# Optimization experiments

Measured on AMD Instinct MI355X. Metric: run time of the kernel, lower is better.

## Reference

```python
import jax, jax.numpy as jnp
import numpy as np

N = 4096   # num nodes
D = 512    # hidden_dim
H = 8      # head_num (hardcoded in module)
E = 131072 # num relation pairs
DH = D // H


def setup_inputs() -> dict:
    key = jax.random.key(0)
    k1, k2, k3, k4, k5, k6 = jax.random.split(key, 6)
    inst_feature = jax.random.normal(k1, (N, D), jnp.float32)
    aggregator_matrix = jax.random.randint(k2, (N, N), 0, 2).astype(jnp.float32)
    # unique (sub, obj) pairs to avoid nondeterministic duplicate scatter-set
    rng = np.random.default_rng(0)
    flat = rng.choice(N * N, size=E, replace=False)
    rel_pair_index = jnp.stack(
        [jnp.asarray(flat // N, jnp.int32), jnp.asarray(flat % N, jnp.int32)], axis=1)
    std = np.sqrt(2.0 / (D + DH)).astype(np.float32)
    w_q = jax.random.normal(k3, (D, D), jnp.float32) * std
    w_k = jax.random.normal(k4, (D, D), jnp.float32) * std
    bnd = 1.0 / np.sqrt(D)
    b_q = jax.random.uniform(k5, (D,), jnp.float32, -bnd, bnd)
    b_k = jax.random.uniform(k6, (D,), jnp.float32, -bnd, bnd)
    return {"inst_feature": inst_feature, "aggregator_matrix": aggregator_matrix,
            "rel_pair_index": rel_pair_index, "w_q": w_q, "b_q": b_q,
            "w_k": w_k, "b_k": b_k}


def reference(inst_feature, aggregator_matrix, rel_pair_index, w_q, b_q, w_k, b_k):
    n, d = inst_feature.shape
    sub = rel_pair_index[:, 0]
    obj = rel_pair_index[:, 1]
    # gather + project (eval mode: dropouts are identity)
    q = (inst_feature[sub] @ w_q.T + b_q).reshape(-1, H, DH)  # [E,H,dh]
    k = (inst_feature[obj] @ w_k.T + b_k).reshape(-1, H, DH)  # [E,H,dh]
    scores = (q * k).sum(-1) / np.sqrt(DH).astype(np.float32)  # [E,H]
    # scatter into dense [H,N,N]
    af = jnp.zeros((H, n, n), inst_feature.dtype).at[:, sub, obj].set(scores.T)
    # mask where aggregator_matrix == 0 (applied before diagonal override)
    af = jnp.where((aggregator_matrix == 0)[None], -jnp.inf, af)
    diag = jnp.arange(n)
    af = af.at[:, diag, diag].set(1e-7)
    p = jax.nn.softmax(af, axis=2)          # softmax over last dim
    factor = p.sum(axis=0) / H              # [N,N]
    return factor @ inst_feature            # [N,D]
```

## Files before the change

### kernel.cpp

```cpp
#include <hip/hip_runtime.h>

#define N_INST 4096
#define D_FEAT 512
#define NHEAD 8
#define NPAIR 131072

typedef __attribute__((ext_vector_type(8))) short short8;
typedef __attribute__((ext_vector_type(4))) float f32x4;
typedef __attribute__((ext_vector_type(4))) unsigned short u16x4;

__device__ inline unsigned short f2bf(float f) {
  union { float f; unsigned u; } v; v.f = f;
  unsigned r = v.u + 0x7fffu + ((v.u >> 16) & 1u);
  return (unsigned short)(r >> 16);
}
__device__ inline float bf2f(unsigned short b) {
  union { unsigned u; float f; } v; v.u = ((unsigned)b) << 16; return v.f;
}
__device__ inline void gload16(const void* g, void* l) {
  __builtin_amdgcn_global_load_lds((const __attribute__((address_space(1))) unsigned int*)g,
                                   (__attribute__((address_space(3))) unsigned int*)l, 16, 0, 0);
}

__global__ __launch_bounds__(256) void k_castw(const float* __restrict__ wq,
                                               const float* __restrict__ wk,
                                               unsigned short* __restrict__ dst) {
  const float* src = blockIdx.y ? wk : wq;
  unsigned short* d = dst + (size_t)blockIdx.y * D_FEAT * D_FEAT;
  int i = (blockIdx.x * 256 + threadIdx.x) * 4;
  float4 v = *(const float4*)&src[i];
  ushort4 o;
  o.x = f2bf(v.x); o.y = f2bf(v.y); o.z = f2bf(v.z); o.w = f2bf(v.w);
  *(ushort4*)&d[i] = o;
}

__global__ __launch_bounds__(256) void k_xprep(const float* __restrict__ x,
                                               unsigned short* __restrict__ xb,
                                               unsigned short* __restrict__ xT) {
  __shared__ float t[32][33];
  int bx = blockIdx.x, by = blockIdx.y;
  int tx = threadIdx.x & 31, ty = threadIdx.x >> 5;
  #pragma unroll
  for (int r = 0; r < 4; ++r) {
    int row = by * 32 + ty + r * 8;
    float v = x[(size_t)row * D_FEAT + bx * 32 + tx];
    t[ty + r * 8][tx] = v;
    xb[(size_t)row * D_FEAT + bx * 32 + tx] = f2bf(v);
  }
  __syncthreads();
  #pragma unroll
  for (int r = 0; r < 4; ++r)
    xT[(size_t)(bx * 32 + ty + r * 8) * N_INST + by * 32 + tx] = f2bf(t[tx][ty + r * 8]);
}

__global__ __launch_bounds__(256) void k_mask_acnt(const float* __restrict__ agg,
                                                   unsigned short* __restrict__ maskb,
                                                   int* __restrict__ acnt) {
  int i = blockIdx.x;
  const f32x4* row = (const f32x4*)(agg + (size_t)i * N_INST);
  u16x4* mrow = (u16x4*)(maskb + (size_t)i * N_INST);
  int tid = threadIdx.x;
  f32x4 v[4];
  #pragma unroll
  for (int u = 0; u < 4; ++u)
    v[u] = __builtin_nontemporal_load(&row[u * 256 + tid]);
  int cnt = 0;
  #pragma unroll
  for (int u = 0; u < 4; ++u) {
    int t = u * 256 + tid;
    u16x4 m;
    m[0] = (v[u][0] != 0.f) ? 0x3F80 : 0;
    m[1] = (v[u][1] != 0.f) ? 0x3F80 : 0;
    m[2] = (v[u][2] != 0.f) ? 0x3F80 : 0;
    m[3] = (v[u][3] != 0.f) ? 0x3F80 : 0;
    cnt += (v[u][0] != 0.f) + (v[u][1] != 0.f) + (v[u][2] != 0.f) + (v[u][3] != 0.f);
    int j = t * 4;
    if (i >= j && i < j + 4) {
      int d = i - j;
      m[d] = 0x3F80;
      cnt -= (v[u][d] != 0.f);
    }
    __builtin_nontemporal_store(m, &mrow[t]);
  }
  #pragma unroll
  for (int msk = 1; msk < 64; msk <<= 1) cnt += __shfl_xor(cnt, msk);
  __shared__ int wsum[4];
  if ((threadIdx.x & 63) == 0) wsum[threadIdx.x >> 6] = cnt;
  __syncthreads();
  if (threadIdx.x == 0) acnt[i] = wsum[0] + wsum[1] + wsum[2] + wsum[3];
}

template<int BIAS, int CBF16, int BN>
__global__ __launch_bounds__(256, 2) void k_gemm(const unsigned short* __restrict__ A,
                                                 const unsigned short* __restrict__ B,
                                                 const float* __restrict__ bias0,
                                                 const float* __restrict__ bias1,
                                                 void* __restrict__ Cv,
                                                 int M, int N, int K, int klen) {
  constexpr int NI = BN / 32;
  constexpr int BCH = BN / 32;
  __shared__ __align__(16) unsigned short lA[2][128 * 64];
  __shared__ __align__(16) unsigned short lB[2][BN * 64];
  int tid = threadIdx.x, wave = tid >> 6, lane = tid & 63;
  int wm = wave & 1, wn = wave >> 1;
  int gx = gridDim.x;
  int nxy = gx * gridDim.y;
  int lin = blockIdx.x + gx * blockIdx.y;
  int nch = nxy >> 3;
  int nl = (lin & 7) * nch + (lin >> 3);
  int bx = nl % gx, by = nl / gx;
  int bm = by * 128, bn = bx * BN;
  int kbase = blockIdx.z * klen;
  int srow = lane >> 3;
  int sg = (lane & 7) ^ srow;
  const unsigned short* ag[4];
  const unsigned short* bg[BCH];
  #pragma unroll
  for (int p = 0; p < 4; ++p) {
    int row = (wave * 4 + p) * 8 + srow;
    ag[p] = A + (size_t)(bm + row) * K + kbase + sg * 8;
  }
  #pragma unroll
  for (int p = 0; p < BCH; ++p) {
    int row = (wave * BCH + p) * 8 + srow;
    bg[p] = B + (size_t)(bn + row) * K + kbase + sg * 8;
  }
  auto stage = [&](int buf) {
    #pragma unroll
    for (int p = 0; p < 4; ++p) { gload16(ag[p], &lA[buf][(wave * 4 + p) * 512]); ag[p] += 64; }
    #pragma unroll
    for (int p = 0; p < BCH; ++p) { gload16(bg[p], &lB[buf][(wave * BCH + p) * 512]); bg[p] += 64; }
  };
  f32x4 acc[4][NI] = {};
  int nt = klen / 64;
  stage(0);
  __syncthreads();
  int cur = 0;
  int lrow = lane & 15, glq = lane >> 4;
  for (int t = 0; t < nt; ++t) {
    if (t + 1 < nt) stage(cur ^ 1);
    short8 bf[2][NI];
    #pragma unroll
    for (int kk = 0; kk < 2; ++kk)
      #pragma unroll
      for (int ni = 0; ni < NI; ++ni) {
        int row = wn * (BN / 2) + ni * 16 + lrow;
        int pg = (kk * 4 + glq) ^ (row & 7);
        bf[kk][ni] = *(const short8*)&lB[cur][row * 64 + pg * 8];
      }
    #pragma unroll
    for (int mi = 0; mi < 4; ++mi)
      #pragma unroll
      for (int kk = 0; kk < 2; ++kk) {
        int row = wm * 64 + mi * 16 + lrow;
        int pg = (kk * 4 + glq) ^ (row & 7);
        short8 af = *(const short8*)&lA[cur][row * 64 + pg * 8];
        #pragma unroll
        for (int ni = 0; ni < NI; ++ni)
          acc[mi][ni] = __builtin_amdgcn_mfma_f32_16x16x32_bf16(af, bf[kk][ni], acc[mi][ni], 0, 0, 0);
      }
    __syncthreads();
    cur ^= 1;
  }
  #pragma unroll
  for (int mi = 0; mi < 4; ++mi)
    #pragma unroll
    for (int ni = 0; ni < NI; ++ni) {
      int col = bn + wn * (BN / 2) + ni * 16 + lrow;
      float bv = 0.f;
      if (BIAS) bv = (col < 512) ? bias0[col] : bias1[col - 512];
      #pragma unroll
      for (int j = 0; j < 4; ++j) {
        int row = bm + wm * 64 + mi * 16 + glq * 4 + j;
        float vv = acc[mi][ni][j] + bv;
        if (CBF16) {
          ((unsigned short*)Cv)[(size_t)row * N + col] = f2bf(vv);
        } else {
          float* C = (float*)Cv + (size_t)blockIdx.z * M * N;
          C[(size_t)row * N + col] = vv;
        }
      }
    }
}

__global__ __launch_bounds__(256) void k_scores(const unsigned short* __restrict__ QKb,
                                                const int* __restrict__ pairs,
                                                const float* __restrict__ agg,
                                                float* __restrict__ es,
                                                float* __restrict__ sumexp,
                                                int* __restrict__ scnt) {
  int wave = threadIdx.x >> 6, lane = threadIdx.x & 63;
  int e = blockIdx.x * 4 + wave;
  int sub = pairs[2 * e], obj = pairs[2 * e + 1];
  short8 q8 = *(const short8*)&QKb[(size_t)sub * 1024 + lane * 8];
  short8 k8 = *(const short8*)&QKb[(size_t)obj * 1024 + 512 + lane * 8];
  float p = 0.f;
  #pragma unroll
  for (int j = 0; j < 8; ++j)
    p += bf2f((unsigned short)q8[j]) * bf2f((unsigned short)k8[j]);
  p += __shfl_xor(p, 1);
  p += __shfl_xor(p, 2);
  p += __shfl_xor(p, 4);
  float ev = expf(p * 0.125f);
  bool valid = (sub != obj) && (agg[(size_t)sub * N_INST + obj] != 0.f);
  int h = lane >> 3;
  if ((lane & 7) == 0) {
    es[(size_t)e * 8 + h] = valid ? ev : -1.f;
    if (valid) atomicAdd(&sumexp[sub * 8 + h], ev);
  }
  if (lane == 0 && valid) atomicAdd(&scnt[sub], 1);
}

__global__ __launch_bounds__(256) void k_denom(const float* __restrict__ sumexp,
                                               const int* __restrict__ scnt,
                                               const int* __restrict__ acnt,
                                               float* __restrict__ invden,
                                               float* __restrict__ base) {
  int i = blockIdx.x * 256 + threadIdx.x;
  if (i >= N_INST) return;
  float c0 = (float)(acnt[i] - scnt[i]);
  const float E0 = expf(1e-7f);
  float bsum = 0.f;
  #pragma unroll
  for (int h = 0; h < NHEAD; ++h) {
    float inv = 1.0f / (E0 + c0 + sumexp[i * NHEAD + h]);
    invden[i * NHEAD + h] = inv;
    bsum += inv;
  }
  base[i] = bsum * (1.0f / NHEAD);
}

__global__ __launch_bounds__(256) void k_scatter(const int* __restrict__ pairs,
                                                 const float* __restrict__ es,
                                                 const float* __restrict__ invden,
                                                 const float* __restrict__ base,
                                                 unsigned short* __restrict__ maskb) {
  int e = blockIdx.x * 256 + threadIdx.x;
  if (e >= NPAIR) return;
  float4 e0 = *(const float4*)&es[(size_t)e * 8];
  if (e0.x < 0.f) return;
  float4 e1 = *(const float4*)&es[(size_t)e * 8 + 4];
  int sub = pairs[2 * e], obj = pairs[2 * e + 1];
  const float* inv = &invden[sub * 8];
  float f = e0.x * inv[0] + e0.y * inv[1] + e0.z * inv[2] + e0.w * inv[3] +
            e1.x * inv[4] + e1.y * inv[5] + e1.z * inv[6] + e1.w * inv[7];
  maskb[(size_t)sub * N_INST + obj] = f2bf(f * 0.125f / base[sub]);
}

__global__ __launch_bounds__(256) void k_redscale(const float* __restrict__ P,
                                                  const float* __restrict__ base,
                                                  float* __restrict__ out) {
  size_t idx = ((size_t)blockIdx.x * 256 + threadIdx.x) * 4;
  int i = (int)(idx >> 9);
  const size_t S = (size_t)N_INST * 512;
  float4 a = *(const float4*)&P[idx];
  float4 b = *(const float4*)&P[idx + S];
  float4 c = *(const float4*)&P[idx + 2 * S];
  float4 d = *(const float4*)&P[idx + 3 * S];
  float s = base[i];
  float4 o;
  o.x = s * (a.x + b.x + c.x + d.x);
  o.y = s * (a.y + b.y + c.y + d.y);
  o.z = s * (a.z + b.z + c.z + d.z);
  o.w = s * (a.w + b.w + c.w + d.w);
  *(float4*)&out[idx] = o;
}

extern "C" void kernel_launch(void* const* d_in, const int* in_sizes, int n_in,
                              void* d_out, int out_size, void* d_ws, size_t ws_size,
                              hipStream_t stream) {
  const float* x   = (const float*)d_in[0];
  const float* agg = (const float*)d_in[1];
  const int*   prs = (const int*)d_in[2];
  const float* w_q = (const float*)d_in[3];
  const float* b_q = (const float*)d_in[4];
  const float* w_k = (const float*)d_in[5];
  const float* b_k = (const float*)d_in[6];
  float* out = (float*)d_out;

  char* ws = (char*)d_ws;
  size_t off = 0;
  auto alloc = [&](size_t bytes) -> void* {
    void* p = ws + off;
    off += (bytes + 255) & ~(size_t)255;
    return p;
  };
  unsigned short* xb    = (unsigned short*)alloc((size_t)N_INST * D_FEAT * 2);
  unsigned short* xbT   = (unsigned short*)alloc((size_t)D_FEAT * N_INST * 2);
  unsigned short* wqkb  = (unsigned short*)alloc((size_t)1024 * D_FEAT * 2);
  void*           QKP   = alloc((size_t)N_INST * 512 * 4 * 4);
  float*          es    = (float*)alloc((size_t)NPAIR * NHEAD * 4);
  float*          sumexp= (float*)alloc((size_t)N_INST * NHEAD * 4);
  int*            scnt  = (int*)alloc((size_t)N_INST * 4);
  int*            acnt  = (int*)alloc((size_t)N_INST * 4);
  float*          invden= (float*)alloc((size_t)N_INST * NHEAD * 4);
  float*          base  = (float*)alloc((size_t)N_INST * 4);
  unsigned short* maskb = (unsigned short*)alloc((size_t)N_INST * N_INST * 2);

  hipMemsetAsync(sumexp, 0, (size_t)N_INST * NHEAD * 4, stream);
  hipMemsetAsync(scnt, 0, (size_t)N_INST * 4, stream);

  k_castw<<<dim3(D_FEAT * D_FEAT / 4 / 256, 2), 256, 0, stream>>>(w_q, w_k, wqkb);
  k_xprep<<<dim3(D_FEAT / 32, N_INST / 32), 256, 0, stream>>>(x, xb, xbT);
  k_mask_acnt<<<dim3(N_INST), 256, 0, stream>>>(agg, maskb, acnt);

  k_gemm<1, 1, 64><<<dim3(1024 / 64, N_INST / 128, 1), 256, 0, stream>>>(
      xb, wqkb, b_q, b_k, QKP, N_INST, 1024, D_FEAT, D_FEAT);

  k_scores<<<dim3(NPAIR / 4), 256, 0, stream>>>((const unsigned short*)QKP, prs, agg, es, sumexp, scnt);
  k_denom<<<dim3(N_INST / 256), 256, 0, stream>>>(sumexp, scnt, acnt, invden, base);
  k_scatter<<<dim3(NPAIR / 256), 256, 0, stream>>>(prs, es, invden, base, maskb);

  k_gemm<0, 0, 128><<<dim3(512 / 128, N_INST / 128, 4), 256, 0, stream>>>(
      maskb, xbT, nullptr, nullptr, QKP, N_INST, 512, N_INST, N_INST / 4);

  k_redscale<<<dim3(N_INST * 512 / 4 / 256), 256, 0, stream>>>((const float*)QKP, base, out);
}
```

Measured before the change: 125.0 us.

## Batch eight pairs per wave in scores and store split-K partials as bf16

The scores kernel now has each wave handle eight pairs. It loads all pair indices and the mask checks up front and issues the Q/K gathers together for more memory-level parallelism. It also skips gathers for masked pairs. Separately, the split-K aggregation GEMM writes its partial sums in bf16 instead of fp32, halving partial-buffer traffic for the reduction kernel. The cost is a precision loss on the partial sums before the final reduction and scaling.

```diff
diff --git a/kernel.cpp b/kernel.cpp
--- a/kernel.cpp
+++ b/kernel.cpp
@@ -174,7 +174,8 @@
         int row = bm + wm * 64 + mi * 16 + glq * 4 + j;
         float vv = acc[mi][ni][j] + bv;
         if (CBF16) {
-          ((unsigned short*)Cv)[(size_t)row * N + col] = f2bf(vv);
+          unsigned short* C = (unsigned short*)Cv + (size_t)blockIdx.z * M * N;
+          C[(size_t)row * N + col] = f2bf(vv);
         } else {
           float* C = (float*)Cv + (size_t)blockIdx.z * M * N;
           C[(size_t)row * N + col] = vv;
@@ -190,25 +191,46 @@
                                                 float* __restrict__ sumexp,
                                                 int* __restrict__ scnt) {
   int wave = threadIdx.x >> 6, lane = threadIdx.x & 63;
-  int e = blockIdx.x * 4 + wave;
-  int sub = pairs[2 * e], obj = pairs[2 * e + 1];
-  short8 q8 = *(const short8*)&QKb[(size_t)sub * 1024 + lane * 8];
-  short8 k8 = *(const short8*)&QKb[(size_t)obj * 1024 + 512 + lane * 8];
-  float p = 0.f;
-  #pragma unroll
-  for (int j = 0; j < 8; ++j)
-    p += bf2f((unsigned short)q8[j]) * bf2f((unsigned short)k8[j]);
-  p += __shfl_xor(p, 1);
-  p += __shfl_xor(p, 2);
-  p += __shfl_xor(p, 4);
-  float ev = expf(p * 0.125f);
-  bool valid = (sub != obj) && (agg[(size_t)sub * N_INST + obj] != 0.f);
-  int h = lane >> 3;
-  if ((lane & 7) == 0) {
-    es[(size_t)e * 8 + h] = valid ? ev : -1.f;
-    if (valid) atomicAdd(&sumexp[sub * 8 + h], ev);
-  }
-  if (lane == 0 && valid) atomicAdd(&scnt[sub], 1);
+  int ebase = (blockIdx.x * 4 + wave) * 8;
+  int subs[8], objs[8];
+  #pragma unroll
+  for (int u = 0; u < 8; ++u) {
+    int2 pr = *(const int2*)&pairs[2 * (ebase + u)];
+    subs[u] = pr.x; objs[u] = pr.y;
+  }
+  bool val[8];
+  #pragma unroll
+  for (int u = 0; u < 8; ++u)
+    val[u] = (subs[u] != objs[u]) && (agg[(size_t)subs[u] * N_INST + objs[u]] != 0.f);
+  short8 q8[8], k8[8];
+  #pragma unroll
+  for (int u = 0; u < 8; ++u) {
+    if (val[u]) {
+      q8[u] = *(const short8*)&QKb[(size_t)subs[u] * 1024 + lane * 8];
+      k8[u] = *(const short8*)&QKb[(size_t)objs[u] * 1024 + 512 + lane * 8];
+    }
+  }
+  #pragma unroll
+  for (int u = 0; u < 8; ++u) {
+    if (!val[u]) {
+      if (lane == 0) es[(size_t)(ebase + u) * 8] = -1.f;
+      continue;
+    }
+    float p = 0.f;
+    #pragma unroll
+    for (int j = 0; j < 8; ++j)
+      p += bf2f((unsigned short)q8[u][j]) * bf2f((unsigned short)k8[u][j]);
+    p += __shfl_xor(p, 1);
+    p += __shfl_xor(p, 2);
+    p += __shfl_xor(p, 4);
+    float ev = expf(p * 0.125f);
+    if ((lane & 7) == 0) {
+      int h = lane >> 3;
+      es[(size_t)(ebase + u) * 8 + h] = ev;
+      atomicAdd(&sumexp[subs[u] * 8 + h], ev);
+    }
+    if (lane == 0) atomicAdd(&scnt[subs[u]], 1);
+  }
 }
 
 __global__ __launch_bounds__(256) void k_denom(const float* __restrict__ sumexp,
@@ -247,22 +269,22 @@
   maskb[(size_t)sub * N_INST + obj] = f2bf(f * 0.125f / base[sub]);
 }
 
-__global__ __launch_bounds__(256) void k_redscale(const float* __restrict__ P,
+__global__ __launch_bounds__(256) void k_redscale(const unsigned short* __restrict__ P,
                                                   const float* __restrict__ base,
                                                   float* __restrict__ out) {
   size_t idx = ((size_t)blockIdx.x * 256 + threadIdx.x) * 4;
   int i = (int)(idx >> 9);
   const size_t S = (size_t)N_INST * 512;
-  float4 a = *(const float4*)&P[idx];
-  float4 b = *(const float4*)&P[idx + S];
-  float4 c = *(const float4*)&P[idx + 2 * S];
-  float4 d = *(const float4*)&P[idx + 3 * S];
+  u16x4 a = *(const u16x4*)&P[idx];
+  u16x4 b = *(const u16x4*)&P[idx + S];
+  u16x4 c = *(const u16x4*)&P[idx + 2 * S];
+  u16x4 d = *(const u16x4*)&P[idx + 3 * S];
   float s = base[i];
   float4 o;
-  o.x = s * (a.x + b.x + c.x + d.x);
-  o.y = s * (a.y + b.y + c.y + d.y);
-  o.z = s * (a.z + b.z + c.z + d.z);
-  o.w = s * (a.w + b.w + c.w + d.w);
+  o.x = s * (bf2f(a[0]) + bf2f(b[0]) + bf2f(c[0]) + bf2f(d[0]));
+  o.y = s * (bf2f(a[1]) + bf2f(b[1]) + bf2f(c[1]) + bf2f(d[1]));
+  o.z = s * (bf2f(a[2]) + bf2f(b[2]) + bf2f(c[2]) + bf2f(d[2]));
+  o.w = s * (bf2f(a[3]) + bf2f(b[3]) + bf2f(c[3]) + bf2f(d[3]));
   *(float4*)&out[idx] = o;
 }
 
@@ -288,7 +310,7 @@
   unsigned short* xb    = (unsigned short*)alloc((size_t)N_INST * D_FEAT * 2);
   unsigned short* xbT   = (unsigned short*)alloc((size_t)D_FEAT * N_INST * 2);
   unsigned short* wqkb  = (unsigned short*)alloc((size_t)1024 * D_FEAT * 2);
-  void*           QKP   = alloc((size_t)N_INST * 512 * 4 * 4);
+  void*           QKP   = alloc((size_t)N_INST * 512 * 2 * 4);
   float*          es    = (float*)alloc((size_t)NPAIR * NHEAD * 4);
   float*          sumexp= (float*)alloc((size_t)N_INST * NHEAD * 4);
   int*            scnt  = (int*)alloc((size_t)N_INST * 4);
@@ -307,12 +329,12 @@
   k_gemm<1, 1, 64><<<dim3(1024 / 64, N_INST / 128, 1), 256, 0, stream>>>(
       xb, wqkb, b_q, b_k, QKP, N_INST, 1024, D_FEAT, D_FEAT);
 
-  k_scores<<<dim3(NPAIR / 4), 256, 0, stream>>>((const unsigned short*)QKP, prs, agg, es, sumexp, scnt);
+  k_scores<<<dim3(NPAIR / 32), 256, 0, stream>>>((const unsigned short*)QKP, prs, agg, es, sumexp, scnt);
   k_denom<<<dim3(N_INST / 256), 256, 0, stream>>>(sumexp, scnt, acnt, invden, base);
   k_scatter<<<dim3(NPAIR / 256), 256, 0, stream>>>(prs, es, invden, base, maskb);
 
-  k_gemm<0, 0, 128><<<dim3(512 / 128, N_INST / 128, 4), 256, 0, stream>>>(
+  k_gemm<0, 1, 128><<<dim3(512 / 128, N_INST / 128, 4), 256, 0, stream>>>(
       maskb, xbT, nullptr, nullptr, QKP, N_INST, 512, N_INST, N_INST / 4);
 
-  k_redscale<<<dim3(N_INST * 512 / 4 / 256), 256, 0, stream>>>((const float*)QKP, base, out);
-}
+  k_redscale<<<dim3(N_INST * 512 / 4 / 256), 256, 0, stream>>>((const unsigned short*)QKP, base, out);
+}
```

Result: no change. 125.2 us (+0.2%).
